# Performance work log

Measured on AMD Instinct MI355X. Metric: run time of the kernel, lower is better.

The kernel has to match this reference:

```python
import jax, jax.numpy as jnp
import numpy as np

N_NODES, IN_DIM = 200000, 512
B, N1, N2 = 1024, 25, 10
D1, D2 = 128, 128
NUM_CLASSES = 41


def _linear_params(key, fan_in, fan_out):
    kw, kb = jax.random.split(key)
    bound = 1.0 / np.sqrt(fan_in)
    W = jax.random.uniform(kw, (fan_in, fan_out), jnp.float32, -bound, bound)
    b = jax.random.uniform(kb, (fan_out,), jnp.float32, -bound, bound)
    return W, b


def setup_inputs() -> dict:
    key = jax.random.key(0)
    ks = jax.random.split(key, 10)
    features = jax.random.normal(ks[0], (N_NODES, IN_DIM), jnp.float32)
    ids0 = jax.random.randint(ks[1], (B,), 0, N_NODES)
    ids1 = jax.random.randint(ks[2], (B * N1,), 0, N_NODES)
    ids2 = jax.random.randint(ks[3], (B * N1 * N2,), 0, N_NODES)
    W2s, b2s = _linear_params(ks[4], IN_DIM, D2)
    W2n, b2n = _linear_params(ks[5], IN_DIM, D2)
    W1s, b1s = _linear_params(ks[6], IN_DIM, D1)
    W1n, b1n = _linear_params(ks[7], 2 * D2, D1)
    Wfc, bfc = _linear_params(ks[8], 2 * D1, NUM_CLASSES)
    return {"features": features, "ids0": ids0, "ids1": ids1, "ids2": ids2,
            "W2s": W2s, "b2s": b2s, "W2n": W2n, "b2n": b2n,
            "W1s": W1s, "b1s": b1s, "W1n": W1n, "b1n": b1n,
            "Wfc": Wfc, "bfc": bfc}


def reference(features, ids0, ids1, ids2, W2s, b2s, W2n, b2n, W1s, b1s, W1n, b1n, Wfc, bfc):
    f0 = features[ids0]   # [B, D]
    f1 = features[ids1]   # [B*n1, D]
    f2 = features[ids2]   # [B*n1*n2, D]
    D = features.shape[1]
    # Faithful to torch: view([B*n1, D, n2]).mean(-1) (original layout quirk)
    agg2 = f2.reshape(f1.shape[0], D, -1).mean(axis=-1)            # [B*n1, D]
    h2 = jax.nn.relu(jnp.concatenate([f1 @ W2s + b2s, agg2 @ W2n + b2n], axis=1))  # [B*n1, 2*d2]
    agg1 = h2.reshape(f0.shape[0], h2.shape[1], -1).mean(axis=-1)  # [B, 2*d2]
    h1 = jnp.concatenate([f0 @ W1s + b1s, agg1 @ W1n + b1n], axis=-1)  # [B, 2*d1]
    return h1 @ Wfc + bfc  # [B, num_classes]
```

## Files before the change

### kernel.cpp

```cpp
#include <hip/hip_runtime.h>
#include <hip/hip_bf16.h>

typedef __attribute__((ext_vector_type(8))) short short8;
typedef __attribute__((ext_vector_type(4))) float floatx4;

__device__ __forceinline__ unsigned short f2b(float f) {
    union { float f; unsigned int u; } v; v.f = f;
    unsigned int u = v.u;
    return (unsigned short)((u + 0x7FFFu + ((u >> 16) & 1u)) >> 16);
}
__device__ __forceinline__ float b2f(unsigned short h) {
    union { unsigned int u; float f; } v; v.u = ((unsigned int)h) << 16;
    return v.f;
}

__global__ __launch_bounds__(256) void agg2_kernel(
    const float* __restrict__ feat, const int* __restrict__ ids2,
    unsigned short* __restrict__ agg2)
{
    __shared__ __align__(16) float buf[5120];
    __shared__ int sid[10];
    const int i = blockIdx.x;
    const int t = threadIdx.x;
    if (t < 10) sid[t] = ids2[i * 10 + t];
    __syncthreads();
#pragma unroll
    for (int p = 0; p < 5; ++p) {
        int q = p * 1024 + t * 4;
        int row = q >> 9, col = q & 511;
        *(float4*)&buf[q] = *(const float4*)&feat[(long)sid[row] * 512 + col];
    }
    __syncthreads();
#pragma unroll
    for (int h = 0; h < 2; ++h) {
        int d = t + h * 256;
        float s = 0.f;
#pragma unroll
        for (int j = 0; j < 10; ++j) s += buf[d * 10 + j];
        agg2[(long)i * 512 + d] = f2b(s * 0.1f);
    }
}

template<bool GATHER, bool RELU>
__global__ __launch_bounds__(256) void gemm_node(
    const void* __restrict__ Asrc, const int* __restrict__ ids,
    const float* __restrict__ W, const float* __restrict__ bias,
    unsigned short* __restrict__ out, int K, int lda, int colbase)
{
    __shared__ __align__(16) unsigned short A_s[64 * 40];
    __shared__ __align__(16) unsigned short B_s[4 * 128 * 8];
    __shared__ int s_ids[64];

    const int t   = threadIdx.x;
    const int m0  = blockIdx.x * 64;
    if (GATHER && t < 64) s_ids[t] = ids[m0 + t];

    const int lane = t & 63;
    const int w    = t >> 6;
    const int q4   = lane >> 4;
    const int l16  = lane & 15;

    floatx4 acc[8];
#pragma unroll
    for (int i = 0; i < 8; ++i) acc[i] = (floatx4){0.f, 0.f, 0.f, 0.f};

    const int r   = t >> 2;
    const int kk  = (t & 3) * 8;
    const int nB  = t & 127;
    const int kb2 = t >> 7;

    if (GATHER) __syncthreads();

    for (int k0 = 0; k0 < K; k0 += 32) {
        if (GATHER) {
            const float* fp = (const float*)Asrc + (long)s_ids[r] * lda + (k0 + kk);
            float4 v1 = *(const float4*)fp;
            float4 v2 = *(const float4*)(fp + 4);
            union { unsigned short us[8]; uint4 v; } tmp;
            tmp.us[0] = f2b(v1.x); tmp.us[1] = f2b(v1.y);
            tmp.us[2] = f2b(v1.z); tmp.us[3] = f2b(v1.w);
            tmp.us[4] = f2b(v2.x); tmp.us[5] = f2b(v2.y);
            tmp.us[6] = f2b(v2.z); tmp.us[7] = f2b(v2.w);
            *(uint4*)&A_s[r * 40 + kk] = tmp.v;
        } else {
            const unsigned short* ap =
                (const unsigned short*)Asrc + (long)(m0 + r) * lda + (k0 + kk);
            *(uint4*)&A_s[r * 40 + kk] = *(const uint4*)ap;
        }
#pragma unroll
        for (int kb = kb2; kb < 4; kb += 2) {
            union { unsigned short us[8]; uint4 v; } tmp;
#pragma unroll
            for (int j = 0; j < 8; ++j)
                tmp.us[j] = f2b(W[(long)(k0 + kb * 8 + j) * 128 + nB]);
            *(uint4*)&B_s[(kb * 128 + nB) * 8] = tmp.v;
        }
        __syncthreads();
        short8 av = *(const short8*)&A_s[(w * 16 + l16) * 40 + q4 * 8];
#pragma unroll
        for (int nt = 0; nt < 8; ++nt) {
            short8 bv = *(const short8*)&B_s[(q4 * 128 + nt * 16 + l16) * 8];
            acc[nt] = __builtin_amdgcn_mfma_f32_16x16x32_bf16(av, bv, acc[nt], 0, 0, 0);
        }
        __syncthreads();
    }
#pragma unroll
    for (int nt = 0; nt < 8; ++nt) {
        int col = nt * 16 + l16;
        float bv = bias[col];
#pragma unroll
        for (int reg = 0; reg < 4; ++reg) {
            int rowl = w * 16 + q4 * 4 + reg;
            float v = acc[nt][reg] + bv;
            if (RELU) v = fmaxf(v, 0.f);
            out[(long)(m0 + rowl) * 256 + colbase + col] = f2b(v);
        }
    }
}

__global__ __launch_bounds__(256) void agg1_kernel(
    const unsigned short* __restrict__ h2, unsigned short* __restrict__ agg1)
{
    __shared__ float buf[6400];
    const int b = blockIdx.x, t = threadIdx.x;
#pragma unroll
    for (int p = 0; p < 25; ++p) {
        int idx = p * 256 + t;
        buf[idx] = b2f(h2[(long)b * 6400 + idx]);
    }
    __syncthreads();
    float s = 0.f;
#pragma unroll
    for (int j = 0; j < 25; ++j) s += buf[t * 25 + j];
    agg1[(long)b * 256 + t] = f2b(s * 0.04f);
}

__global__ __launch_bounds__(64) void fc_kernel(
    const unsigned short* __restrict__ h1, const float* __restrict__ Wfc,
    const float* __restrict__ bfc, float* __restrict__ out)
{
    __shared__ float row[256];
    const int b = blockIdx.x, t = threadIdx.x;
#pragma unroll
    for (int p = 0; p < 4; ++p) row[p * 64 + t] = b2f(h1[(long)b * 256 + p * 64 + t]);
    __syncthreads();
    if (t < 41) {
        float s = bfc[t];
        for (int k = 0; k < 256; ++k) s += row[k] * Wfc[k * 41 + t];
        out[(long)b * 41 + t] = s;
    }
}

extern "C" void kernel_launch(void* const* d_in, const int* in_sizes, int n_in,
                              void* d_out, int out_size, void* d_ws, size_t ws_size,
                              hipStream_t stream) {
    const float* features = (const float*)d_in[0];
    const int*   ids0     = (const int*)d_in[1];
    const int*   ids1     = (const int*)d_in[2];
    const int*   ids2     = (const int*)d_in[3];
    const float* W2s      = (const float*)d_in[4];
    const float* b2s      = (const float*)d_in[5];
    const float* W2n      = (const float*)d_in[6];
    const float* b2n      = (const float*)d_in[7];
    const float* W1s      = (const float*)d_in[8];
    const float* b1s      = (const float*)d_in[9];
    const float* W1n      = (const float*)d_in[10];
    const float* b1n      = (const float*)d_in[11];
    const float* Wfc      = (const float*)d_in[12];
    const float* bfc      = (const float*)d_in[13];
    float* out = (float*)d_out;

    char* ws = (char*)d_ws;
    unsigned short* agg2b = (unsigned short*)(ws);
    unsigned short* h2b   = (unsigned short*)(ws + 26214400);
    unsigned short* agg1b = (unsigned short*)(ws + 39321600);
    unsigned short* h1b   = (unsigned short*)(ws + 39845888);

    agg2_kernel<<<25600, 256, 0, stream>>>(features, ids2, agg2b);
    gemm_node<true,  true ><<<400, 256, 0, stream>>>(features, ids1, W2s, b2s, h2b, 512, 512, 0);
    gemm_node<false, true ><<<400, 256, 0, stream>>>(agg2b,  nullptr, W2n, b2n, h2b, 512, 512, 128);
    agg1_kernel<<<1024, 256, 0, stream>>>(h2b, agg1b);
    gemm_node<true,  false><<<16, 256, 0, stream>>>(features, ids0, W1s, b1s, h1b, 512, 512, 0);
    gemm_node<false, false><<<16, 256, 0, stream>>>(agg1b, nullptr, W1n, b1n, h1b, 256, 256, 128);
    fc_kernel<<<1024, 64, 0, stream>>>(h1b, Wfc, bfc, out);
}
```

Measured before the change: 672.4 us.

## Pre-convert weights to bf16 fragments and merge independent GEMM/aggregation launches

Adds a prep kernel that converts the four weight matrices to bf16 in the MFMA fragment layout once per call. The GEMMs then load B tiles directly into LDS with global_load_lds instead of converting fp32 weights in every block. The self-feature GEMM for hop-1 now shares a launch with the agg2 gather kernel, and the two final small GEMMs are merged into one launch with 32-row tiles, which doubles the block count there. This removes repeated per-block weight conversion and some launch overhead, but adds an extra prep launch plus scratch writes.

```diff
diff --git a/kernel.cpp b/kernel.cpp
--- a/kernel.cpp
+++ b/kernel.cpp
@@ -4,113 +4,107 @@
 typedef __attribute__((ext_vector_type(8))) short short8;
 typedef __attribute__((ext_vector_type(4))) float floatx4;
 
-__device__ __forceinline__ unsigned short f2b(float f) {
+static __device__ __forceinline__ unsigned short f2b(float f) {
     union { float f; unsigned int u; } v; v.f = f;
     unsigned int u = v.u;
     return (unsigned short)((u + 0x7FFFu + ((u >> 16) & 1u)) >> 16);
 }
-__device__ __forceinline__ float b2f(unsigned short h) {
+static __device__ __forceinline__ float b2f(unsigned short h) {
     union { unsigned int u; float f; } v; v.u = ((unsigned int)h) << 16;
     return v.f;
 }
 
-__global__ __launch_bounds__(256) void agg2_kernel(
-    const float* __restrict__ feat, const int* __restrict__ ids2,
-    unsigned short* __restrict__ agg2)
-{
-    __shared__ __align__(16) float buf[5120];
-    __shared__ int sid[10];
-    const int i = blockIdx.x;
+#define GLDS16(gp, lp)                                                         \
+    __builtin_amdgcn_global_load_lds(                                          \
+        (const __attribute__((address_space(1))) unsigned int*)(gp),           \
+        (__attribute__((address_space(3))) unsigned int*)(lp), 16, 0, 0)
+
+__global__ __launch_bounds__(256) void prep_w(
+    const float* __restrict__ W2s, const float* __restrict__ W2n,
+    const float* __restrict__ W1s, const float* __restrict__ W1n,
+    unsigned short* __restrict__ F2s, unsigned short* __restrict__ F2n,
+    unsigned short* __restrict__ F1s, unsigned short* __restrict__ F1n)
+{
+    const int b = blockIdx.x, t = threadIdx.x;
+    const float* src; unsigned short* dst; int o;
+    if (b < 256)      { src = W2s; dst = F2s; o = b * 256 + t; }
+    else if (b < 512) { src = W2n; dst = F2n; o = (b - 256) * 256 + t; }
+    else if (b < 768) { src = W1s; dst = F1s; o = (b - 512) * 256 + t; }
+    else              { src = W1n; dst = F1n; o = (b - 768) * 256 + t; }
+    const int k8 = o & 7, n = (o >> 3) & 127, kb = (o >> 10) & 3, kb32 = o >> 12;
+    const int k = kb32 * 32 + kb * 8 + k8;
+    dst[o] = f2b(src[k * 128 + n]);
+}
+
+template<int BM, bool GATHER, bool RELU>
+__device__ __forceinline__ void gemm_body(
+    const void* __restrict__ Asrc, const int* __restrict__ ids,
+    const unsigned short* __restrict__ Wfrag, const float* __restrict__ bias,
+    unsigned short* __restrict__ out, int K, int lda, int colbase, int m0,
+    unsigned short* A_s , unsigned short* B_s , int* s_ids)
+{
     const int t = threadIdx.x;
-    if (t < 10) sid[t] = ids2[i * 10 + t];
-    __syncthreads();
-#pragma unroll
-    for (int p = 0; p < 5; ++p) {
-        int q = p * 1024 + t * 4;
-        int row = q >> 9, col = q & 511;
-        *(float4*)&buf[q] = *(const float4*)&feat[(long)sid[row] * 512 + col];
-    }
-    __syncthreads();
-#pragma unroll
-    for (int h = 0; h < 2; ++h) {
-        int d = t + h * 256;
-        float s = 0.f;
-#pragma unroll
-        for (int j = 0; j < 10; ++j) s += buf[d * 10 + j];
-        agg2[(long)i * 512 + d] = f2b(s * 0.1f);
-    }
-}
-
-template<bool GATHER, bool RELU>
-__global__ __launch_bounds__(256) void gemm_node(
-    const void* __restrict__ Asrc, const int* __restrict__ ids,
-    const float* __restrict__ W, const float* __restrict__ bias,
-    unsigned short* __restrict__ out, int K, int lda, int colbase)
-{
-    __shared__ __align__(16) unsigned short A_s[64 * 40];
-    __shared__ __align__(16) unsigned short B_s[4 * 128 * 8];
-    __shared__ int s_ids[64];
-
-    const int t   = threadIdx.x;
-    const int m0  = blockIdx.x * 64;
-    if (GATHER && t < 64) s_ids[t] = ids[m0 + t];
+    if (GATHER && t < BM) s_ids[t] = ids[m0 + t];
 
     const int lane = t & 63;
     const int w    = t >> 6;
     const int q4   = lane >> 4;
     const int l16  = lane & 15;
 
-    floatx4 acc[8];
-#pragma unroll
-    for (int i = 0; i < 8; ++i) acc[i] = (floatx4){0.f, 0.f, 0.f, 0.f};
-
-    const int r   = t >> 2;
-    const int kk  = (t & 3) * 8;
-    const int nB  = t & 127;
-    const int kb2 = t >> 7;
+    const int wm  = (BM == 64) ? w * 16 : (w & 1) * 16;
+    const int wn0 = (BM == 64) ? 0      : (w >> 1) * 64;
+    constexpr int NT = (BM == 64) ? 8 : 4;
+
+    floatx4 acc[NT];
+#pragma unroll
+    for (int i = 0; i < NT; ++i) acc[i] = (floatx4){0.f, 0.f, 0.f, 0.f};
+
+    const int r  = t >> 2;
+    const int kk = (t & 3) * 8;
 
     if (GATHER) __syncthreads();
 
-    for (int k0 = 0; k0 < K; k0 += 32) {
-        if (GATHER) {
-            const float* fp = (const float*)Asrc + (long)s_ids[r] * lda + (k0 + kk);
-            float4 v1 = *(const float4*)fp;
-            float4 v2 = *(const float4*)(fp + 4);
-            union { unsigned short us[8]; uint4 v; } tmp;
-            tmp.us[0] = f2b(v1.x); tmp.us[1] = f2b(v1.y);
-            tmp.us[2] = f2b(v1.z); tmp.us[3] = f2b(v1.w);
-            tmp.us[4] = f2b(v2.x); tmp.us[5] = f2b(v2.y);
-            tmp.us[6] = f2b(v2.z); tmp.us[7] = f2b(v2.w);
-            *(uint4*)&A_s[r * 40 + kk] = tmp.v;
-        } else {
-            const unsigned short* ap =
-                (const unsigned short*)Asrc + (long)(m0 + r) * lda + (k0 + kk);
-            *(uint4*)&A_s[r * 40 + kk] = *(const uint4*)ap;
-        }
-#pragma unroll
-        for (int kb = kb2; kb < 4; kb += 2) {
-            union { unsigned short us[8]; uint4 v; } tmp;
-#pragma unroll
-            for (int j = 0; j < 8; ++j)
-                tmp.us[j] = f2b(W[(long)(k0 + kb * 8 + j) * 128 + nB]);
-            *(uint4*)&B_s[(kb * 128 + nB) * 8] = tmp.v;
-        }
-        __syncthreads();
-        short8 av = *(const short8*)&A_s[(w * 16 + l16) * 40 + q4 * 8];
-#pragma unroll
-        for (int nt = 0; nt < 8; ++nt) {
-            short8 bv = *(const short8*)&B_s[(q4 * 128 + nt * 16 + l16) * 8];
+    const int nkb = K >> 5;
+    for (int kb32 = 0; kb32 < nkb; ++kb32) {
+        const int k0 = kb32 * 32;
+        if (BM == 64 || t < 128) {
+            if (GATHER) {
+                const float* fp = (const float*)Asrc + (long)s_ids[r] * lda + (k0 + kk);
+                float4 v1 = *(const float4*)fp;
+                float4 v2 = *(const float4*)(fp + 4);
+                union { unsigned short us[8]; uint4 v; } tmp;
+                tmp.us[0] = f2b(v1.x); tmp.us[1] = f2b(v1.y);
+                tmp.us[2] = f2b(v1.z); tmp.us[3] = f2b(v1.w);
+                tmp.us[4] = f2b(v2.x); tmp.us[5] = f2b(v2.y);
+                tmp.us[6] = f2b(v2.z); tmp.us[7] = f2b(v2.w);
+                *(uint4*)&A_s[r * 40 + kk] = tmp.v;
+            } else {
+                const unsigned short* ap =
+                    (const unsigned short*)Asrc + (long)(m0 + r) * lda + (k0 + kk);
+                *(uint4*)&A_s[r * 40 + kk] = *(const uint4*)ap;
+            }
+        }
+        {
+            const char* gb = (const char*)Wfrag + (size_t)kb32 * 8192 + (size_t)lane * 16;
+            GLDS16(gb + (w * 2 + 0) * 1024, (char*)B_s + (w * 2 + 0) * 1024);
+            GLDS16(gb + (w * 2 + 1) * 1024, (char*)B_s + (w * 2 + 1) * 1024);
+        }
+        __syncthreads();
+        short8 av = *(const short8*)&A_s[(wm + l16) * 40 + q4 * 8];
+#pragma unroll
+        for (int nt = 0; nt < NT; ++nt) {
+            short8 bv = *(const short8*)&B_s[(q4 * 128 + wn0 + nt * 16 + l16) * 8];
             acc[nt] = __builtin_amdgcn_mfma_f32_16x16x32_bf16(av, bv, acc[nt], 0, 0, 0);
         }
         __syncthreads();
     }
 #pragma unroll
-    for (int nt = 0; nt < 8; ++nt) {
-        int col = nt * 16 + l16;
-        float bv = bias[col];
+    for (int nt = 0; nt < NT; ++nt) {
+        const int col = wn0 + nt * 16 + l16;
+        const float bv = bias[col];
 #pragma unroll
         for (int reg = 0; reg < 4; ++reg) {
-            int rowl = w * 16 + q4 * 4 + reg;
+            const int rowl = wm + q4 * 4 + reg;
             float v = acc[nt][reg] + bv;
             if (RELU) v = fmaxf(v, 0.f);
             out[(long)(m0 + rowl) * 256 + colbase + col] = f2b(v);
@@ -118,6 +112,56 @@
     }
 }
 
+__global__ __launch_bounds__(256) void fused_agg2_gemm(
+    const float* __restrict__ feat, const int* __restrict__ ids2,
+    unsigned short* __restrict__ agg2, const int* __restrict__ ids1,
+    const unsigned short* __restrict__ F2s, const float* __restrict__ b2s,
+    unsigned short* __restrict__ h2)
+{
+    __shared__ __align__(16) char smem[20736];
+    const int b = blockIdx.x;
+    const int t = threadIdx.x;
+    if (b < 400) {
+        unsigned short* A_s = (unsigned short*)smem;
+        unsigned short* B_s = (unsigned short*)(smem + 5120);
+        int* s_ids = (int*)(smem + 13312);
+        gemm_body<64, true, true>(feat, ids1, F2s, b2s, h2, 512, 512, 0,
+                                  b * 64, A_s, B_s, s_ids);
+    } else {
+        float* buf = (float*)smem;
+        int* sid = (int*)(smem + 20480);
+        const int i = b - 400;
+        if (t < 10) sid[t] = ids2[i * 10 + t];
+        __syncthreads();
+#pragma unroll
+        for (int p = 0; p < 5; ++p) {
+            int q = p * 1024 + t * 4;
+            int row = q >> 9, col = q & 511;
+            *(float4*)&buf[q] = *(const float4*)&feat[(long)sid[row] * 512 + col];
+        }
+        __syncthreads();
+#pragma unroll
+        for (int h = 0; h < 2; ++h) {
+            int d = t + h * 256;
+            float s = 0.f;
+#pragma unroll
+            for (int j = 0; j < 10; ++j) s += buf[d * 10 + j];
+            agg2[(long)i * 512 + d] = f2b(s * 0.1f);
+        }
+    }
+}
+
+__global__ __launch_bounds__(256) void gemm_n2(
+    const unsigned short* __restrict__ agg2b, const unsigned short* __restrict__ F2n,
+    const float* __restrict__ b2n, unsigned short* __restrict__ h2)
+{
+    __shared__ __align__(16) unsigned short A_s[64 * 40];
+    __shared__ __align__(16) unsigned short B_s[4096];
+    __shared__ int s_ids[64];
+    gemm_body<64, false, true>(agg2b, nullptr, F2n, b2n, h2, 512, 512, 128,
+                               blockIdx.x * 64, A_s, B_s, s_ids);
+}
+
 __global__ __launch_bounds__(256) void agg1_kernel(
     const unsigned short* __restrict__ h2, unsigned short* __restrict__ agg1)
 {
@@ -133,6 +177,25 @@
 #pragma unroll
     for (int j = 0; j < 25; ++j) s += buf[t * 25 + j];
     agg1[(long)b * 256 + t] = f2b(s * 0.04f);
+}
+
+__global__ __launch_bounds__(256) void tail_gemm(
+    const float* __restrict__ feat, const int* __restrict__ ids0,
+    const unsigned short* __restrict__ agg1b,
+    const unsigned short* __restrict__ F1s, const unsigned short* __restrict__ F1n,
+    const float* __restrict__ b1s, const float* __restrict__ b1n,
+    unsigned short* __restrict__ h1)
+{
+    __shared__ __align__(16) unsigned short A_s[32 * 40];
+    __shared__ __align__(16) unsigned short B_s[4096];
+    __shared__ int s_ids[32];
+    const int b = blockIdx.x;
+    if (b < 32)
+        gemm_body<32, true, false>(feat, ids0, F1s, b1s, h1, 512, 512, 0,
+                                   b * 32, A_s, B_s, s_ids);
+    else
+        gemm_body<32, false, false>(agg1b, nullptr, F1n, b1n, h1, 256, 256, 128,
+                                    (b - 32) * 32, A_s, B_s, s_ids);
 }
 
 __global__ __launch_bounds__(64) void fc_kernel(
@@ -175,12 +238,15 @@
     unsigned short* h2b   = (unsigned short*)(ws + 26214400);
     unsigned short* agg1b = (unsigned short*)(ws + 39321600);
     unsigned short* h1b   = (unsigned short*)(ws + 39845888);
-
-    agg2_kernel<<<25600, 256, 0, stream>>>(features, ids2, agg2b);
-    gemm_node<true,  true ><<<400, 256, 0, stream>>>(features, ids1, W2s, b2s, h2b, 512, 512, 0);
-    gemm_node<false, true ><<<400, 256, 0, stream>>>(agg2b,  nullptr, W2n, b2n, h2b, 512, 512, 128);
+    unsigned short* F2s   = (unsigned short*)(ws + 40370176);
+    unsigned short* F2n   = (unsigned short*)(ws + 40501248);
+    unsigned short* F1s   = (unsigned short*)(ws + 40632320);
+    unsigned short* F1n   = (unsigned short*)(ws + 40763392);
+
+    prep_w<<<896, 256, 0, stream>>>(W2s, W2n, W1s, W1n, F2s, F2n, F1s, F1n);
+    fused_agg2_gemm<<<26000, 256, 0, stream>>>(features, ids2, agg2b, ids1, F2s, b2s, h2b);
+    gemm_n2<<<400, 256, 0, stream>>>(agg2b, F2n, b2n, h2b);
     agg1_kernel<<<1024, 256, 0, stream>>>(h2b, agg1b);
-    gemm_node<true,  false><<<16, 256, 0, stream>>>(features, ids0, W1s, b1s, h1b, 512, 512, 0);
-    gemm_node<false, false><<<16, 256, 0, stream>>>(agg1b, nullptr, W1n, b1n, h1b, 256, 256, 128);
+    tail_gemm<<<64, 256, 0, stream>>>(features, ids0, agg1b, F1s, F1n, b1s, b1n, h1b);
     fc_kernel<<<1024, 64, 0, stream>>>(h1b, Wfc, bfc, out);
 }
```

New measurement: 618.0 us. 1.09x faster.
